# Kernel optimization log

Hardware: AMD Instinct MI355X
Metric: run time of the kernel (lower is better)

## Reference

```python
import jax, jax.numpy as jnp
import numpy as np

N_VISITS, N_PROC, N_MED = 64, 32, 16
V_DIAG, V_PROC, V_MED = 2000, 1500, 4000
EMB, EMB_FF = 256, 128


def _normalize(adj):
    # row-normalize(adj + I), matching GCN.normalize
    adj = adj + np.eye(adj.shape[0], dtype=np.float32)
    rs = adj.sum(1)
    rinv = np.where(rs > 0, 1.0 / rs, 0.0).astype(np.float32)
    return (adj * rinv[:, None]).astype(np.float32)


def setup_inputs() -> dict:
    key = jax.random.key(0)
    ks = jax.random.split(key, 24)
    rng = np.random.default_rng(0)
    ehr = (rng.random((V_MED, V_MED)) < 0.01).astype(np.float32)
    ddi = (rng.random((V_MED, V_MED)) < 0.01).astype(np.float32)
    s = 0.02
    return {
        'proc_codes': jax.random.randint(ks[0], (N_VISITS, N_PROC), 0, V_DIAG + V_PROC + 2),
        'med_codes': jax.random.randint(ks[1], (N_VISITS, N_MED), 0, V_MED),
        'emb_table': jax.random.normal(ks[2], (V_DIAG + V_PROC + 2, EMB_FF)) * s,
        'conv_w': jax.random.normal(ks[3], (3,)) * 0.3,
        'conv_b': jnp.zeros((1,)),
        'wq': jax.random.normal(ks[4], (EMB_FF, EMB)) * s,
        'wk': jax.random.normal(ks[5], (EMB_FF, EMB)) * s,
        'wv': jax.random.normal(ks[6], (EMB_FF, EMB)) * s,
        'wr': jax.random.normal(ks[7], (EMB, EMB)) * s,
        'alpha': jax.random.normal(ks[8], (EMB,)),
        'beta': jax.random.normal(ks[9], (EMB,)),
        'ehr_adj_norm': jnp.asarray(_normalize(ehr)),
        'ddi_adj_norm': jnp.asarray(_normalize(ddi)),
        'ddi_adj_raw': jnp.asarray(ddi),
        'ehr_w1': jax.random.normal(ks[10], (V_MED, EMB)) * s,
        'ehr_b1': jnp.zeros((EMB,)),
        'ehr_w2': jax.random.normal(ks[11], (EMB, EMB)) * s,
        'ehr_b2': jnp.zeros((EMB,)),
        'ddi_w1': jax.random.normal(ks[12], (V_MED, EMB)) * s,
        'ddi_b1': jnp.zeros((EMB,)),
        'ddi_w2': jax.random.normal(ks[13], (EMB, EMB)) * s,
        'ddi_b2': jnp.zeros((EMB,)),
        'inter': jax.random.normal(ks[14], (1,)) * 0.1,
        'out_w1': jax.random.normal(ks[15], (3 * EMB, 2 * EMB)) * s,
        'out_b1': jnp.zeros((2 * EMB,)),
        'out_w2': jax.random.normal(ks[16], (2 * EMB, V_MED)) * s,
        'out_b2': jnp.zeros((V_MED,)),
    }


def _fastformer(x, wq, wk, wv, wr, alpha, beta):
    # x: (1, n, EMB_FF); additive linear attention (all-ones mask => no-op)
    q = x @ wq  # (1, n, EMB)
    k = x @ wk
    v = x @ wv
    scale = EMB ** -0.5
    aw = jax.nn.softmax(q * alpha * scale, axis=-1)
    gq = jnp.sum(q * aw, axis=1)              # global query (1, EMB)
    p = gq[:, None, :] * k                    # (1, n, EMB)
    bw = jax.nn.softmax(p * beta * scale, axis=-1)
    gk = jnp.sum(p * bw, axis=1)              # global key (1, EMB)
    return (gk[:, None, :] * v) @ wr + q


def _gcn(adj, w1, b1, w2, b2):
    # input x = I, so first layer support is just w1
    h = jax.nn.relu(adj @ w1 + b1)
    return adj @ (h @ w2) + b2


def reference(proc_codes, med_codes, emb_table, conv_w, conv_b, wq, wk, wv, wr, alpha, beta,
              ehr_adj_norm, ddi_adj_norm, ddi_adj_raw,
              ehr_w1, ehr_b1, ehr_w2, ehr_b2, ddi_w1, ddi_b1, ddi_w2, ddi_b2,
              inter, out_w1, out_b1, out_w2, out_b2):
    n = proc_codes.shape[0]
    # per-admission mean embedding  (n, EMB_FF)
    i2 = emb_table[proc_codes].mean(axis=1)
    # Conv1d(1,1,k=3,same) over the feature dim, then ReLU
    xp = jnp.pad(i2, ((0, 0), (1, 1)))
    i2 = jax.nn.relu(conv_w[0] * xp[:, :-2] + conv_w[1] * xp[:, 1:-1] + conv_w[2] * xp[:, 2:] + conv_b)
    feat = _fastformer(i2[None], wq, wk, wv, wr, alpha, beta)[0]  # (n, EMB)
    query = feat[-1:]
    drug_memory = _gcn(ehr_adj_norm, ehr_w1, ehr_b1, ehr_w2, ehr_b2) \
        - _gcn(ddi_adj_norm, ddi_w1, ddi_b1, ddi_w2, ddi_b2) * inter[0]
    key_w1 = jax.nn.softmax(query @ drug_memory.T, axis=-1)   # (1, V_MED)
    fact1 = key_w1 @ drug_memory                              # (1, EMB)
    # history (len(input) > 1): multi-hot med history values
    history_keys = feat[:-1]
    hv = jnp.zeros((n - 1, V_MED), dtype=feat.dtype)
    hv = hv.at[jnp.arange(n - 1)[:, None], med_codes[:-1]].set(1.0)
    visit_w = jax.nn.softmax(query @ history_keys.T, axis=-1)
    fact2 = (visit_w @ hv) @ drug_memory
    h = jnp.concatenate([query, fact1, fact2], axis=-1)       # (1, 3*EMB)
    result = jax.nn.relu(h @ out_w1 + out_b1) @ out_w2 + out_b2
    sp = jax.nn.sigmoid(result)[0]
    batch_neg = 0.0005 * jnp.einsum('i,ij,j->', sp, ddi_adj_raw, sp)
    return result, batch_neg
```

## Files before the change

### kernel.cpp

```cpp
#include <hip/hip_runtime.h>
#include <hip/hip_bf16.h>

#define NV 64
#define NP 32
#define NM 16
#define VMED 4000
#define EMB 256
#define EMBFF 128
#define CAP 128


__device__ __forceinline__ float block_sum_256(float v, float* red) {
    int t = threadIdx.x;
    red[t] = v; __syncthreads();
    for (int s = 128; s > 0; s >>= 1) { if (t < s) red[t] += red[t + s]; __syncthreads(); }
    float r = red[0]; __syncthreads();
    return r;
}
__device__ __forceinline__ float block_max_256(float v, float* red) {
    int t = threadIdx.x;
    red[t] = v; __syncthreads();
    for (int s = 128; s > 0; s >>= 1) { if (t < s) red[t] = fmaxf(red[t], red[t + s]); __syncthreads(); }
    float r = red[0]; __syncthreads();
    return r;
}

__global__ void k_ff1(const int* __restrict__ proc, const float* __restrict__ emb,
                      const float* __restrict__ cw, const float* __restrict__ cb,
                      const float* __restrict__ wq, const float* __restrict__ wk,
                      const float* __restrict__ wv, const float* __restrict__ alpha,
                      float* __restrict__ q, float* __restrict__ k, float* __restrict__ v,
                      float* __restrict__ qaw) {
    __shared__ float sm[EMBFF + 2];
    __shared__ float x[EMBFF];
    __shared__ float red[256];
    int vi = blockIdx.x, t = threadIdx.x;
    if (t < EMBFF) {
        float s = 0.f;
        for (int c = 0; c < NP; c++) s += emb[proc[vi * NP + c] * EMBFF + t];
        sm[t + 1] = s * (1.0f / NP);
    }
    if (t == 0) { sm[0] = 0.f; sm[EMBFF + 1] = 0.f; }
    __syncthreads();
    if (t < EMBFF) {
        float o = cw[0] * sm[t] + cw[1] * sm[t + 1] + cw[2] * sm[t + 2] + cb[0];
        x[t] = o > 0.f ? o : 0.f;
    }
    __syncthreads();
    float aq = 0, ak = 0, av = 0;
    for (int e = 0; e < EMBFF; e++) {
        float xe = x[e];
        aq += xe * wq[e * EMB + t];
        ak += xe * wk[e * EMB + t];
        av += xe * wv[e * EMB + t];
    }
    q[vi * EMB + t] = aq; k[vi * EMB + t] = ak; v[vi * EMB + t] = av;
    const float scale = 0.0625f;
    float z = aq * alpha[t] * scale;
    float m = block_max_256(z, red);
    float e_ = __expf(z - m);
    float sum = block_sum_256(e_, red);
    qaw[vi * EMB + t] = aq * (e_ / sum);
}

__global__ void k_pbw(const float* __restrict__ qaw, const float* __restrict__ k,
                      const float* __restrict__ beta, float* __restrict__ pbw) {
    __shared__ float red[256];
    int vi = blockIdx.x, f = threadIdx.x;
    float g = 0;
    for (int r = 0; r < NV; r++) g += qaw[r * EMB + f];
    float p = g * k[vi * EMB + f];
    const float scale = 0.0625f;
    float z = p * beta[f] * scale;
    float m = block_max_256(z, red);
    float e_ = __expf(z - m);
    float sum = block_sum_256(e_, red);
    pbw[vi * EMB + f] = p * (e_ / sum);
}

__global__ void k_feat(const float* __restrict__ pbw, const float* __restrict__ v,
                       const float* __restrict__ q, const float* __restrict__ wr,
                       float* __restrict__ feat) {
    __shared__ float s[EMB];
    int vi = blockIdx.x, f = threadIdx.x;
    float g = 0;
    for (int r = 0; r < NV; r++) g += pbw[r * EMB + f];
    s[f] = g * v[vi * EMB + f];
    __syncthreads();
    float acc = 0;
    for (int e = 0; e < EMB; e++) acc += s[e] * wr[e * EMB + f];
    feat[vi * EMB + f] = acc + q[vi * EMB + f];
}

__global__ void k_visitw_wmed(const float* __restrict__ feat, const int* __restrict__ med,
                              float* __restrict__ w_med) {
    __shared__ float qs[EMB];
    __shared__ float vw[64];
    __shared__ float red[256];
    __shared__ float wm[VMED];
    int t = threadIdx.x;
    for (int e = t; e < EMB; e += 256) qs[e] = feat[63 * EMB + e];
    for (int i = t; i < VMED; i += 256) wm[i] = 0.f;
    __syncthreads();
    float sc = -1e30f;
    if (t < 63) {
        float a = 0;
        for (int e = 0; e < EMB; e++) a += qs[e] * feat[t * EMB + e];
        sc = a;
    }
    float m = block_max_256(sc, red);
    float e_ = (t < 63) ? __expf(sc - m) : 0.f;
    float sum = block_sum_256(e_, red);
    if (t < 63) vw[t] = e_ / sum;
    __syncthreads();
    for (int i = t; i < 63 * NM; i += 256) {
        int vv = i / NM, mm = i % NM;
        int code = med[vv * NM + mm];
        bool dup = false;
        for (int m2 = 0; m2 < mm; m2++)
            if (med[vv * NM + m2] == code) dup = true;
        if (!dup) atomicAdd(&wm[code], vw[vv]);
    }
    __syncthreads();
    for (int i = t; i < VMED; i += 256) w_med[i] = wm[i];
}

__global__ void k_scan(const float* __restrict__ eadj, const float* __restrict__ dadj,
                       int* __restrict__ ccntE, int* __restrict__ cidxE, float* __restrict__ cvalE,
                       int* __restrict__ ccntD, int* __restrict__ cidxD, float* __restrict__ cvalD) {
    __shared__ int idx[CAP];
    __shared__ float val[CAP];
    __shared__ int cnt;
    int b = blockIdx.x, t = threadIdx.x;
    bool isD = b >= VMED;
    int i = isD ? b - VMED : b;
    const float* adj = isD ? dadj : eadj;
    int*   ccnt = isD ? ccntD : ccntE;
    int*   cidx = isD ? cidxD : cidxE;
    float* cval = isD ? cvalD : cvalE;
    if (t == 0) cnt = 0;
    __syncthreads();
    const float4* row4 = (const float4*)(adj + (size_t)i * VMED);
    for (int j4 = t; j4 < VMED / 4; j4 += 256) {
        float4 a = row4[j4];
        int c0 = j4 * 4;
        if (a.x != 0.f) { int p = atomicAdd(&cnt, 1); if (p < CAP) { idx[p] = c0;     val[p] = a.x; } }
        if (a.y != 0.f) { int p = atomicAdd(&cnt, 1); if (p < CAP) { idx[p] = c0 + 1; val[p] = a.y; } }
        if (a.z != 0.f) { int p = atomicAdd(&cnt, 1); if (p < CAP) { idx[p] = c0 + 2; val[p] = a.z; } }
        if (a.w != 0.f) { int p = atomicAdd(&cnt, 1); if (p < CAP) { idx[p] = c0 + 3; val[p] = a.w; } }
    }
    __syncthreads();
    int n = cnt < CAP ? cnt : CAP;
    if (t == 0) ccnt[i] = n;
    if (t < n) { cidx[i * CAP + t] = idx[t]; cval[i * CAP + t] = val[t]; }
}

__global__ void k_gcn2(const int* __restrict__ ccntE, const int* __restrict__ cidxE,
                       const float* __restrict__ cvalE,
                       const int* __restrict__ ccntD, const int* __restrict__ cidxD,
                       const float* __restrict__ cvalD,
                       const float* __restrict__ ew1, const float* __restrict__ eb1,
                       const float* __restrict__ ew2,
                       const float* __restrict__ dw1, const float* __restrict__ db1,
                       const float* __restrict__ dw2,
                       float* __restrict__ outE, float* __restrict__ outD) {
    __shared__ float x[8][EMB];
    __shared__ int idx[8][CAP];
    __shared__ float val[8][CAP];
    __shared__ int nn8[8];
    int b = blockIdx.x, t = threadIdx.x;
    bool isD = b >= 500;
    const int*   ccnt = isD ? ccntD : ccntE;
    const int*   cidx = isD ? cidxD : cidxE;
    const float* cval = isD ? cvalD : cvalE;
    const float* w1   = isD ? dw1 : ew1;
    const float* b1   = isD ? db1 : eb1;
    const float* w2   = isD ? dw2 : ew2;
    float* outp = isD ? outD : outE;
    int r0 = (isD ? b - 500 : b) * 8;
    for (int r = 0; r < 8; r++) {
        int n = ccnt[r0 + r];
        int n8 = (n + 7) & ~7;
        if (t == 0) nn8[r] = n8;
        if (t < n) { idx[r][t] = cidx[(r0 + r) * CAP + t]; val[r][t] = cval[(r0 + r) * CAP + t]; }
        else if (t < n8) { idx[r][t] = 0; val[r][t] = 0.f; }
    }
    __syncthreads();
    for (int r = 0; r < 8; r++) {
        float acc = b1[t];
        int n8 = nn8[r];
        for (int e = 0; e < n8; e += 8) {
            float g0 = w1[(size_t)idx[r][e]     * EMB + t];
            float g1 = w1[(size_t)idx[r][e + 1] * EMB + t];
            float g2 = w1[(size_t)idx[r][e + 2] * EMB + t];
            float g3 = w1[(size_t)idx[r][e + 3] * EMB + t];
            float g4 = w1[(size_t)idx[r][e + 4] * EMB + t];
            float g5 = w1[(size_t)idx[r][e + 5] * EMB + t];
            float g6 = w1[(size_t)idx[r][e + 6] * EMB + t];
            float g7 = w1[(size_t)idx[r][e + 7] * EMB + t];
            acc += val[r][e]     * g0 + val[r][e + 1] * g1
                 + val[r][e + 2] * g2 + val[r][e + 3] * g3
                 + val[r][e + 4] * g4 + val[r][e + 5] * g5
                 + val[r][e + 6] * g6 + val[r][e + 7] * g7;
        }
        x[r][t] = acc > 0.f ? acc : 0.f;
    }
    __syncthreads();
    float a[8] = {0, 0, 0, 0, 0, 0, 0, 0};
    #pragma unroll 4
    for (int e = 0; e < EMB; e++) {
        float we = w2[e * EMB + t];
        #pragma unroll
        for (int r = 0; r < 8; r++) a[r] += x[r][e] * we;
    }
    for (int r = 0; r < 8; r++) outp[(size_t)(r0 + r) * EMB + t] = a[r];
}

__global__ void k_acc(const int* __restrict__ ccntE, const int* __restrict__ cidxE,
                      const float* __restrict__ cvalE,
                      const int* __restrict__ ccntD, const int* __restrict__ cidxD,
                      const float* __restrict__ cvalD,
                      const float* __restrict__ xe, const float* __restrict__ xd,
                      const float* __restrict__ b2e, const float* __restrict__ b2d,
                      const float* __restrict__ inter, const float* __restrict__ feat,
                      float* __restrict__ dm, float* __restrict__ sdm) {
    __shared__ int idxE[CAP];
    __shared__ float valE[CAP];
    __shared__ int idxD[CAP];
    __shared__ float valD[CAP];
    __shared__ float red[256];
    int i = blockIdx.x, t = threadIdx.x;
    int nE = ccntE[i], nD = ccntD[i];
    int nE8 = (nE + 7) & ~7, nD8 = (nD + 7) & ~7;
    if (t < nE) { idxE[t] = cidxE[i * CAP + t]; valE[t] = cvalE[i * CAP + t]; }
    else if (t < nE8) { idxE[t] = 0; valE[t] = 0.f; }
    if (t < nD) { idxD[t] = cidxD[i * CAP + t]; valD[t] = cvalD[i * CAP + t]; }
    else if (t < nD8) { idxD[t] = 0; valD[t] = 0.f; }
    __syncthreads();
    float aE = b2e[t];
    for (int e = 0; e < nE8; e += 8) {
        float g0 = xe[(size_t)idxE[e]     * EMB + t];
        float g1 = xe[(size_t)idxE[e + 1] * EMB + t];
        float g2 = xe[(size_t)idxE[e + 2] * EMB + t];
        float g3 = xe[(size_t)idxE[e + 3] * EMB + t];
        float g4 = xe[(size_t)idxE[e + 4] * EMB + t];
        float g5 = xe[(size_t)idxE[e + 5] * EMB + t];
        float g6 = xe[(size_t)idxE[e + 6] * EMB + t];
        float g7 = xe[(size_t)idxE[e + 7] * EMB + t];
        aE += valE[e] * g0 + valE[e + 1] * g1 + valE[e + 2] * g2 + valE[e + 3] * g3
            + valE[e + 4] * g4 + valE[e + 5] * g5 + valE[e + 6] * g6 + valE[e + 7] * g7;
    }
    float aD = b2d[t];
    for (int e = 0; e < nD8; e += 8) {
        float g0 = xd[(size_t)idxD[e]     * EMB + t];
        float g1 = xd[(size_t)idxD[e + 1] * EMB + t];
        float g2 = xd[(size_t)idxD[e + 2] * EMB + t];
        float g3 = xd[(size_t)idxD[e + 3] * EMB + t];
        float g4 = xd[(size_t)idxD[e + 4] * EMB + t];
        float g5 = xd[(size_t)idxD[e + 5] * EMB + t];
        float g6 = xd[(size_t)idxD[e + 6] * EMB + t];
        float g7 = xd[(size_t)idxD[e + 7] * EMB + t];
        aD += valD[e] * g0 + valD[e + 1] * g1 + valD[e + 2] * g2 + valD[e + 3] * g3
            + valD[e + 4] * g4 + valD[e + 5] * g5 + valD[e + 6] * g6 + valD[e + 7] * g7;
    }
    float dmv = aE - inter[0] * aD;
    dm[(size_t)i * EMB + t] = dmv;
    float s = block_sum_256(dmv * feat[63 * EMB + t], red);
    if (t == 0) sdm[i] = s;
}

__global__ void k_softmax4000(const float* __restrict__ s, float* __restrict__ out) {
    __shared__ float red[256];
    int t = threadIdx.x;
    float m = -1e30f;
    for (int i = t; i < VMED; i += 256) m = fmaxf(m, s[i]);
    m = block_max_256(m, red);
    float sum = 0;
    for (int i = t; i < VMED; i += 256) { float e = __expf(s[i] - m); out[i] = e; sum += e; }
    sum = block_sum_256(sum, red);
    float inv = 1.f / sum;
    for (int i = t; i < VMED; i += 256) out[i] *= inv;
}

__global__ void k_facts_part(const float* __restrict__ dm, const float* __restrict__ kw,
                             const float* __restrict__ wm, float* __restrict__ part1,
                             float* __restrict__ part2) {
    int f = threadIdx.x, b = blockIdx.x;
    int r0 = b * 100;
    float a1 = 0, a2 = 0;
    for (int r = r0; r < r0 + 100; r++) {
        float d = dm[(size_t)r * EMB + f];
        a1 += kw[r] * d;
        a2 += wm[r] * d;
    }
    part1[b * EMB + f] = a1;
    part2[b * EMB + f] = a2;
}

__global__ void k_hidden_part(const float* __restrict__ feat, const float* __restrict__ part1,
                              const float* __restrict__ part2, const float* __restrict__ w1,
                              float* __restrict__ hpart) {
    __shared__ float xs[16];
    int b = blockIdx.x, t = threadIdx.x;
    int e0 = b * 16;
    if (t < 16) {
        int e = e0 + t;
        float xv;
        if (e < 256) xv = feat[63 * EMB + e];
        else if (e < 512) { float s = 0; for (int p = 0; p < 40; p++) s += part1[p * EMB + (e - 256)]; xv = s; }
        else              { float s = 0; for (int p = 0; p < 40; p++) s += part2[p * EMB + (e - 512)]; xv = s; }
        xs[t] = xv;
    }
    __syncthreads();
    float a1 = 0, a2 = 0;
    #pragma unroll
    for (int i = 0; i < 16; i++) {
        int e = e0 + i;
        a1 += xs[i] * w1[e * 512 + t];
        a2 += xs[i] * w1[e * 512 + t + 256];
    }
    hpart[b * 512 + t] = a1;
    hpart[b * 512 + t + 256] = a2;
}

__global__ void k_result(const float* __restrict__ hpart, const float* __restrict__ b1,
                         const float* __restrict__ w2, const float* __restrict__ b2,
                         float* __restrict__ out, float* __restrict__ sp) {
    __shared__ float hx[512];
    __shared__ float red[8][32];
    int t = threadIdx.x;
    for (int jj = t; jj < 512; jj += 256) {
        float s = b1[jj];
        for (int p = 0; p < 48; p++) s += hpart[p * 512 + jj];
        hx[jj] = s > 0.f ? s : 0.f;
    }
    __syncthreads();
    int lane = t & 31, seg = t >> 5;
    int j = blockIdx.x * 32 + lane;
    float acc = 0;
    int e0 = seg * 64;
    #pragma unroll 8
    for (int e = e0; e < e0 + 64; e++) acc += hx[e] * w2[(size_t)e * VMED + j];
    red[seg][lane] = acc;
    __syncthreads();
    if (seg == 0) {
        float s = b2[j];
        for (int p = 0; p < 8; p++) s += red[p][lane];
        out[j] = s;
        sp[j] = 1.f / (1.f + __expf(-s));
    }
}

__global__ void k_bneg(const float* __restrict__ ddi, const float* __restrict__ sp,
                       float* __restrict__ bpart) {
    __shared__ float4 spl[VMED / 4];
    __shared__ float red[8][256];
    int t = threadIdx.x;
    const float4* sp4 = (const float4*)sp;
    for (int j4 = t; j4 < VMED / 4; j4 += 256) spl[j4] = sp4[j4];
    __syncthreads();
    int i0 = blockIdx.x * 8;
    const float4* row4 = (const float4*)(ddi + (size_t)i0 * VMED);
    float p[8] = {0, 0, 0, 0, 0, 0, 0, 0};
    for (int j4 = t; j4 < VMED / 4; j4 += 256) {
        float4 s4 = spl[j4];
        #pragma unroll
        for (int rr = 0; rr < 8; rr++) {
            float4 a = row4[rr * (VMED / 4) + j4];
            p[rr] += a.x * s4.x + a.y * s4.y + a.z * s4.z + a.w * s4.w;
        }
    }
    #pragma unroll
    for (int rr = 0; rr < 8; rr++) red[rr][t] = p[rr];
    __syncthreads();
    for (int s = 128; s > 0; s >>= 1) {
        if (t < s) {
            #pragma unroll
            for (int rr = 0; rr < 8; rr++) red[rr][t] += red[rr][t + s];
        }
        __syncthreads();
    }
    if (t < 8) bpart[i0 + t] = sp[i0 + t] * red[t][0];
}

__global__ void FastRx_wo_Diag_19473381720179_kernel(const float* __restrict__ bpart,
                                                     float* __restrict__ out) {
    __shared__ float red[256];
    int t = threadIdx.x;
    float s = 0;
    for (int i = t; i < VMED; i += 256) s += bpart[i];
    s = block_sum_256(s, red);
    if (t == 0) out[VMED] = 0.0005f * s;
}

extern "C" __attribute__((visibility("default")))
void kernel_launch(void* const* d_in, const int* in_sizes, int n_in,
                   void* d_out, int out_size, void* d_ws, size_t ws_size,
                   hipStream_t stream) {
    const int*   proc_codes = (const int*)d_in[0];
    const int*   med_codes  = (const int*)d_in[1];
    const float* emb_table  = (const float*)d_in[2];
    const float* conv_w     = (const float*)d_in[3];
    const float* conv_b     = (const float*)d_in[4];
    const float* wq         = (const float*)d_in[5];
    const float* wk         = (const float*)d_in[6];
    const float* wv         = (const float*)d_in[7];
    const float* wr         = (const float*)d_in[8];
    const float* alpha      = (const float*)d_in[9];
    const float* beta       = (const float*)d_in[10];
    const float* ehr_adj    = (const float*)d_in[11];
    const float* ddi_adj    = (const float*)d_in[12];
    const float* ddi_raw    = (const float*)d_in[13];
    const float* ehr_w1     = (const float*)d_in[14];
    const float* ehr_b1     = (const float*)d_in[15];
    const float* ehr_w2     = (const float*)d_in[16];
    const float* ehr_b2     = (const float*)d_in[17];
    const float* ddi_w1     = (const float*)d_in[18];
    const float* ddi_b1     = (const float*)d_in[19];
    const float* ddi_w2     = (const float*)d_in[20];
    const float* ddi_b2     = (const float*)d_in[21];
    const float* inter      = (const float*)d_in[22];
    const float* out_w1     = (const float*)d_in[23];
    const float* out_b1     = (const float*)d_in[24];
    const float* out_w2     = (const float*)d_in[25];
    const float* out_b2     = (const float*)d_in[26];
    float* out = (float*)d_out;

    float* w = (float*)d_ws;
    float* q      = w;
    float* k      = w + 16384;
    float* v      = w + 32768;
    float* tmpA   = w + 49152;
    float* tmpB   = w + 65536;
    float* feat   = w + 81920;
    float* wmed   = w + 98304;
    float* sdm    = w + 102400;
    float* sp     = w + 106496;
    float* bufA   = w + 110592;
    float* bufC   = bufA + 1024000;
    float* bufB   = bufC + 1024000;
    int*   ccntE  = (int*)(bufB + 1024000);
    int*   cidxE  = ccntE + 4096;
    float* cvalE  = (float*)(cidxE + 512000);
    int*   ccntD  = (int*)(cvalE + 512000);
    int*   cidxD  = ccntD + 4096;
    float* cvalD  = (float*)(cidxD + 512000);
    float* part1  = bufA;
    float* part2  = bufA + 10240;
    float* hpart  = bufA + 20480;
    float* bpart  = bufA + 45056;

    k_ff1<<<NV, EMB, 0, stream>>>(proc_codes, emb_table, conv_w, conv_b,
                                  wq, wk, wv, alpha, q, k, v, tmpA);
    k_pbw<<<NV, EMB, 0, stream>>>(tmpA, k, beta, tmpB);
    k_feat<<<NV, EMB, 0, stream>>>(tmpB, v, q, wr, feat);
    k_visitw_wmed<<<1, 256, 0, stream>>>(feat, med_codes, wmed);

    k_scan<<<2 * VMED, 256, 0, stream>>>(ehr_adj, ddi_adj,
                                         ccntE, cidxE, cvalE, ccntD, cidxD, cvalD);
    k_gcn2<<<1000, 256, 0, stream>>>(ccntE, cidxE, cvalE, ccntD, cidxD, cvalD,
                                     ehr_w1, ehr_b1, ehr_w2,
                                     ddi_w1, ddi_b1, ddi_w2,
                                     bufA, bufC);
    k_acc<<<VMED, 256, 0, stream>>>(ccntE, cidxE, cvalE, ccntD, cidxD, cvalD,
                                    bufA, bufC, ehr_b2, ddi_b2, inter, feat,
                                    bufB, sdm);

    k_softmax4000<<<1, 256, 0, stream>>>(sdm, sdm);
    k_facts_part<<<40, 256, 0, stream>>>(bufB, sdm, wmed, part1, part2);
    k_hidden_part<<<48, 256, 0, stream>>>(feat, part1, part2, out_w1, hpart);
    k_result<<<125, 256, 0, stream>>>(hpart, out_b1, out_w2, out_b2, out, sp);
    k_bneg<<<VMED / 8, 256, 0, stream>>>(ddi_raw, sp, bpart);
    FastRx_wo_Diag_19473381720179_kernel<<<1, 256, 0, stream>>>(bpart, out);
}
```

Before: 412.9 us.

## Halve GCN rows per block, interleave EHR/DDI blocks, split accumulation kernel

k_gcn2 now handles 4 rows per block instead of 8, using 2000 blocks, and interleaves EHR and DDI blocks so neighbouring blocks alternate between the two graphs. The goal is more parallelism and a better balance of L2 use. The fused k_acc is split into k_accE and k_accD, run back to back, so each kernel gathers from only one table at a time. The cost is an extra launch, a write and re-read of dm, and the w2 weight reads being reused across fewer rows per block.

```diff
diff --git a/kernel.cpp b/kernel.cpp
--- a/kernel.cpp
+++ b/kernel.cpp
@@ -164,12 +164,13 @@
                        const float* __restrict__ dw1, const float* __restrict__ db1,
                        const float* __restrict__ dw2,
                        float* __restrict__ outE, float* __restrict__ outD) {
-    __shared__ float x[8][EMB];
-    __shared__ int idx[8][CAP];
-    __shared__ float val[8][CAP];
-    __shared__ int nn8[8];
+    __shared__ float x[4][EMB];
+    __shared__ int idx[4][CAP];
+    __shared__ float val[4][CAP];
+    __shared__ int nn8[4];
     int b = blockIdx.x, t = threadIdx.x;
-    bool isD = b >= 500;
+    bool isD = (b & 4) != 0;
+    int rank = (b >> 3) * 4 + (b & 3);
     const int*   ccnt = isD ? ccntD : ccntE;
     const int*   cidx = isD ? cidxD : cidxE;
     const float* cval = isD ? cvalD : cvalE;
@@ -177,8 +178,8 @@
     const float* b1   = isD ? db1 : eb1;
     const float* w2   = isD ? dw2 : ew2;
     float* outp = isD ? outD : outE;
-    int r0 = (isD ? b - 500 : b) * 8;
-    for (int r = 0; r < 8; r++) {
+    int r0 = rank * 4;
+    for (int r = 0; r < 4; r++) {
         int n = ccnt[r0 + r];
         int n8 = (n + 7) & ~7;
         if (t == 0) nn8[r] = n8;
@@ -186,7 +187,7 @@
         else if (t < n8) { idx[r][t] = 0; val[r][t] = 0.f; }
     }
     __syncthreads();
-    for (int r = 0; r < 8; r++) {
+    for (int r = 0; r < 4; r++) {
         float acc = b1[t];
         int n8 = nn8[r];
         for (int e = 0; e < n8; e += 8) {
@@ -206,36 +207,26 @@
         x[r][t] = acc > 0.f ? acc : 0.f;
     }
     __syncthreads();
-    float a[8] = {0, 0, 0, 0, 0, 0, 0, 0};
+    float a[4] = {0, 0, 0, 0};
     #pragma unroll 4
     for (int e = 0; e < EMB; e++) {
         float we = w2[e * EMB + t];
         #pragma unroll
-        for (int r = 0; r < 8; r++) a[r] += x[r][e] * we;
-    }
-    for (int r = 0; r < 8; r++) outp[(size_t)(r0 + r) * EMB + t] = a[r];
-}
-
-__global__ void k_acc(const int* __restrict__ ccntE, const int* __restrict__ cidxE,
-                      const float* __restrict__ cvalE,
-                      const int* __restrict__ ccntD, const int* __restrict__ cidxD,
-                      const float* __restrict__ cvalD,
-                      const float* __restrict__ xe, const float* __restrict__ xd,
-                      const float* __restrict__ b2e, const float* __restrict__ b2d,
-                      const float* __restrict__ inter, const float* __restrict__ feat,
-                      float* __restrict__ dm, float* __restrict__ sdm) {
+        for (int r = 0; r < 4; r++) a[r] += x[r][e] * we;
+    }
+    for (int r = 0; r < 4; r++) outp[(size_t)(r0 + r) * EMB + t] = a[r];
+}
+
+__global__ void k_accE(const int* __restrict__ ccntE, const int* __restrict__ cidxE,
+                       const float* __restrict__ cvalE, const float* __restrict__ xe,
+                       const float* __restrict__ b2e, float* __restrict__ dm) {
     __shared__ int idxE[CAP];
     __shared__ float valE[CAP];
-    __shared__ int idxD[CAP];
-    __shared__ float valD[CAP];
-    __shared__ float red[256];
     int i = blockIdx.x, t = threadIdx.x;
-    int nE = ccntE[i], nD = ccntD[i];
-    int nE8 = (nE + 7) & ~7, nD8 = (nD + 7) & ~7;
+    int nE = ccntE[i];
+    int nE8 = (nE + 7) & ~7;
     if (t < nE) { idxE[t] = cidxE[i * CAP + t]; valE[t] = cvalE[i * CAP + t]; }
     else if (t < nE8) { idxE[t] = 0; valE[t] = 0.f; }
-    if (t < nD) { idxD[t] = cidxD[i * CAP + t]; valD[t] = cvalD[i * CAP + t]; }
-    else if (t < nD8) { idxD[t] = 0; valD[t] = 0.f; }
     __syncthreads();
     float aE = b2e[t];
     for (int e = 0; e < nE8; e += 8) {
@@ -250,6 +241,23 @@
         aE += valE[e] * g0 + valE[e + 1] * g1 + valE[e + 2] * g2 + valE[e + 3] * g3
             + valE[e + 4] * g4 + valE[e + 5] * g5 + valE[e + 6] * g6 + valE[e + 7] * g7;
     }
+    dm[(size_t)i * EMB + t] = aE;
+}
+
+__global__ void k_accD(const int* __restrict__ ccntD, const int* __restrict__ cidxD,
+                       const float* __restrict__ cvalD, const float* __restrict__ xd,
+                       const float* __restrict__ b2d, const float* __restrict__ inter,
+                       const float* __restrict__ feat, float* __restrict__ dm,
+                       float* __restrict__ sdm) {
+    __shared__ int idxD[CAP];
+    __shared__ float valD[CAP];
+    __shared__ float red[256];
+    int i = blockIdx.x, t = threadIdx.x;
+    int nD = ccntD[i];
+    int nD8 = (nD + 7) & ~7;
+    if (t < nD) { idxD[t] = cidxD[i * CAP + t]; valD[t] = cvalD[i * CAP + t]; }
+    else if (t < nD8) { idxD[t] = 0; valD[t] = 0.f; }
+    __syncthreads();
     float aD = b2d[t];
     for (int e = 0; e < nD8; e += 8) {
         float g0 = xd[(size_t)idxD[e]     * EMB + t];
@@ -263,7 +271,7 @@
         aD += valD[e] * g0 + valD[e + 1] * g1 + valD[e + 2] * g2 + valD[e + 3] * g3
             + valD[e + 4] * g4 + valD[e + 5] * g5 + valD[e + 6] * g6 + valD[e + 7] * g7;
     }
-    float dmv = aE - inter[0] * aD;
+    float dmv = dm[(size_t)i * EMB + t] - inter[0] * aD;
     dm[(size_t)i * EMB + t] = dmv;
     float s = block_sum_256(dmv * feat[63 * EMB + t], red);
     if (t == 0) sdm[i] = s;
@@ -458,13 +466,13 @@
 
     k_scan<<<2 * VMED, 256, 0, stream>>>(ehr_adj, ddi_adj,
                                          ccntE, cidxE, cvalE, ccntD, cidxD, cvalD);
-    k_gcn2<<<1000, 256, 0, stream>>>(ccntE, cidxE, cvalE, ccntD, cidxD, cvalD,
+    k_gcn2<<<2000, 256, 0, stream>>>(ccntE, cidxE, cvalE, ccntD, cidxD, cvalD,
                                      ehr_w1, ehr_b1, ehr_w2,
                                      ddi_w1, ddi_b1, ddi_w2,
                                      bufA, bufC);
-    k_acc<<<VMED, 256, 0, stream>>>(ccntE, cidxE, cvalE, ccntD, cidxD, cvalD,
-                                    bufA, bufC, ehr_b2, ddi_b2, inter, feat,
-                                    bufB, sdm);
+    k_accE<<<VMED, 256, 0, stream>>>(ccntE, cidxE, cvalE, bufA, ehr_b2, bufB);
+    k_accD<<<VMED, 256, 0, stream>>>(ccntD, cidxD, cvalD, bufC, ddi_b2, inter,
+                                     feat, bufB, sdm);
 
     k_softmax4000<<<1, 256, 0, stream>>>(sdm, sdm);
     k_facts_part<<<40, 256, 0, stream>>>(bufB, sdm, wmed, part1, part2);
```

Measured after the change: 407.4 us (median of 2 runs). No clear change (-1.3%).
